# Performance work log

Measured on AMD Instinct MI355X. Metric: run time of the kernel, lower is better.

The kernel has to match this reference:

```python
import jax, jax.numpy as jnp
import numpy as np

B, S, LW = 64, 128, 20
CHAR_V, CHAR_E, CHAR_C = 100, 30, 30
WORD_V, WORD_E = 100000, 300
H, NC = 256, 25
F = WORD_E + CHAR_C  # 330


def setup_inputs() -> dict:
    key = jax.random.key(0)
    ks = jax.random.split(key, 16)
    u = lambda k, shape, s: jax.random.uniform(k, shape, jnp.float32, -s, s)
    sent = jax.random.randint(ks[0], (B, S), 0, WORD_V)
    word = jax.random.randint(ks[1], (B, S, LW), 0, CHAR_V)
    tag = jax.random.randint(ks[2], (B, S), 0, NC)
    lengths = jax.random.randint(ks[3], (B,), S // 2, S + 1)
    mask = jnp.arange(S)[None, :] < lengths[:, None]  # [B,S] bool, mask[:,0] all True

    word_table = u(ks[4], (WORD_V, WORD_E), 0.5)
    char_table = u(ks[5], (CHAR_V, CHAR_E), (3.0 / CHAR_E) ** 0.5)
    conv_w = u(ks[6], (CHAR_C, CHAR_E, 3), (6.0 / (CHAR_E * 3 + CHAR_C)) ** 0.5)
    conv_b = jnp.zeros((CHAR_C,), jnp.float32)

    def lstm_params(k):
        k1, k2 = jax.random.split(k)
        s_ih = (6.0 / (4 * H + F)) ** 0.5
        s_hh = (6.0 / (4 * H + H)) ** 0.5
        w_ih = u(k1, (4 * H, F), s_ih)
        w_hh = u(k2, (4 * H, H), s_hh)
        # b_ih + b_hh, each with forget-gate slice [H:2H] = 1.0 -> combined 2.0
        b = jnp.zeros((4 * H,), jnp.float32).at[H:2 * H].set(2.0)
        return w_ih, w_hh, b

    w_ih_f, w_hh_f, b_f = lstm_params(ks[7])
    w_ih_r, w_hh_r, b_r = lstm_params(ks[8])
    s_lin = (6.0 / (NC + 2 * H)) ** 0.5
    lin_w = u(ks[9], (NC, 2 * H), s_lin)
    lin_b = jnp.zeros((NC,), jnp.float32)
    start_t = u(ks[10], (NC,), 0.1)
    end_t = u(ks[11], (NC,), 0.1)
    trans = u(ks[12], (NC, NC), 0.1)
    return dict(word_table=word_table, char_table=char_table, conv_w=conv_w,
                conv_b=conv_b, w_ih_f=w_ih_f, w_hh_f=w_hh_f, b_f=b_f,
                w_ih_r=w_ih_r, w_hh_r=w_hh_r, b_r=b_r, lin_w=lin_w, lin_b=lin_b,
                start_t=start_t, end_t=end_t, trans=trans,
                sent=sent, word=word, tag=tag, mask=mask)


def _lstm_dir(x, w_ih, w_hh, b, reverse):
    # x: [B,S,F] -> precompute input projections time-major [S,B,4H]
    gx = jnp.einsum('bsf,gf->sbg', x, w_ih) + b
    bsz = x.shape[0]
    hs = w_hh.shape[1]

    def step(carry, g):
        h, c = carry
        g = g + h @ w_hh.T
        i, f, gg, o = jnp.split(g, 4, axis=-1)
        c = jax.nn.sigmoid(f) * c + jax.nn.sigmoid(i) * jnp.tanh(gg)
        h = jax.nn.sigmoid(o) * jnp.tanh(c)
        return (h, c), h

    init = (jnp.zeros((bsz, hs), x.dtype), jnp.zeros((bsz, hs), x.dtype))
    _, hseq = jax.lax.scan(step, init, gx, reverse=reverse)
    return hseq  # [S,B,H]


def _crf_nll(em, tg, mk, start_t, end_t, trans):
    # em: [S,B,C] emissions; tg: [S,B] int; mk: [S,B] float (mk[0]=1)
    bsz = em.shape[1]
    bidx = jnp.arange(bsz)
    # numerator: gold path score
    em_tag = jnp.take_along_axis(em, tg[..., None], axis=-1)[..., 0]   # [S,B]
    tr = trans[tg[:-1], tg[1:]]                                        # [S-1,B]
    score = start_t[tg[0]] + em_tag[0] + jnp.sum(mk[1:] * (tr + em_tag[1:]), axis=0)
    last = mk.sum(0).astype(jnp.int32) - 1
    score = score + end_t[tg[last, bidx]]
    # denominator: forward algorithm (logsumexp scan over time)
    alpha0 = start_t[None, :] + em[0]                                   # [B,C]

    def step(alpha, xs):
        em_t, mk_t = xs
        nxt = jax.nn.logsumexp(alpha[:, :, None] + trans[None, :, :] + em_t[:, None, :], axis=1)
        alpha = jnp.where(mk_t[:, None] > 0, nxt, alpha)
        return alpha, None

    alpha, _ = jax.lax.scan(step, alpha0, (em[1:], mk[1:]))
    logZ = jax.nn.logsumexp(alpha + end_t[None, :], axis=1)
    return -jnp.sum(score - logZ)  # model returns -log_likelihood (reduction='sum')


def reference(word_table, char_table, conv_w, conv_b, w_ih_f, w_hh_f, b_f,
              w_ih_r, w_hh_r, b_r, lin_w, lin_b, start_t, end_t, trans,
              sent, word, tag, mask):
    # --- char CNN encoder (dropout = identity in eval; no ReLU in original forward) ---
    ct = char_table.at[0].set(0.0)                      # padding_idx=0
    cemb = ct[word]                                     # [B,S,LW,E]
    x = cemb.reshape(B * S, LW, CHAR_E).transpose(0, 2, 1)  # [BS,E,LW]
    conv = jax.lax.conv_general_dilated(
        x, conv_w, window_strides=(1,), padding=[(1, 1)],
        dimension_numbers=('NCH', 'OIH', 'NCH')) + conv_b[None, :, None]
    char_feat = conv.max(axis=2).reshape(B, S, CHAR_C)  # global max-pool over chars
    # --- word embedding + concat ---
    wemb = word_table[sent]                             # [B,S,WORD_E]
    feat = jnp.concatenate([wemb, char_feat], axis=2)   # [B,S,F]
    # --- biLSTM ---
    hf = _lstm_dir(feat, w_ih_f, w_hh_f, b_f, reverse=False)
    hr = _lstm_dir(feat, w_ih_r, w_hh_r, b_r, reverse=True)
    h = jnp.concatenate([hf, hr], axis=-1)              # [S,B,2H] time-major
    em = h @ lin_w.T + lin_b                            # [S,B,NC]
    # --- CRF negative log-likelihood ---
    tg = tag.T
    mk = mask.T.astype(em.dtype)
    return _crf_nll(em, tg, mk, start_t, end_t, trans)
```

## Files before the change

### kernel.cpp

```cpp
#include <hip/hip_runtime.h>
#include <math.h>

#define B_  64
#define S_  128
#define LW_ 20
#define CHAR_E_ 30
#define CHAR_C_ 30
#define WORD_E_ 300
#define H_  256
#define NC_ 25
#define F_  330
#define KP_ 352
#define G4_ 1024
#define NG_ 2048

typedef __attribute__((ext_vector_type(8))) short short8;
typedef __attribute__((ext_vector_type(4))) float floatx4;
typedef __attribute__((ext_vector_type(8))) int int8v;

__device__ __forceinline__ unsigned int f2bf(float f){
    unsigned int u = __float_as_uint(f);
    u += 0x7FFFu + ((u>>16)&1u);
    return (u>>16) & 0xFFFFu;
}
__device__ __forceinline__ float bf2f(unsigned int v){ return __uint_as_float(v<<16); }

__device__ __forceinline__ float bfh(uint2 pk, int g){
    unsigned int w = (g < 2) ? pk.x : pk.y;
    return __uint_as_float((g & 1) ? (w & 0xffff0000u) : (w << 16));
}

__device__ __forceinline__ float sigf_(float x){ return __builtin_amdgcn_rcpf(1.0f+__expf(-x)); }
__device__ __forceinline__ float tanhf2_(float x){ return 1.0f - 2.0f*__builtin_amdgcn_rcpf(1.0f+__expf(2.0f*x)); }

__device__ __forceinline__ void gload16(const void* g, void* l){
    __builtin_amdgcn_global_load_lds((const __attribute__((address_space(1))) unsigned int*)g,
                                     (__attribute__((address_space(3))) unsigned int*)l, 16, 0, 0);
}

#define BAR_LDS() __asm__ volatile("s_waitcnt lgkmcnt(0)\n\ts_barrier" ::: "memory")

__global__ __launch_bounds__(256) void k_prep(const float* ct, const int* word,
        const float* cw, const float* cb, const float* wt, const int* sent,
        const float* wf, const float* wr, float* out,
        unsigned short* feat, unsigned short* wpack){
    __shared__ __align__(16) float x[8][32][20];
    int blk = blockIdx.x;
    int tid = threadIdx.x;
    if(blk < 1024){
        int tok0 = blk*8;
        for(int e = tid; e < 8*32*20; e += 256){
            int t  = e % 20;
            int ic = (e/20) & 31;
            int tl = e / 640;
            int id = word[(size_t)(tok0+tl)*LW_ + t];
            float v = 0.f;
            if(ic < CHAR_E_ && id != 0) v = ct[(size_t)id*CHAR_E_ + ic];
            x[tl][ic][t] = v;
        }
        __syncthreads();
        if(tid < 240){
            int tl = tid/30, oc = tid%30;
            float acc[22];
            #pragma unroll
            for(int q=0;q<22;q++) acc[q] = 0.f;
            for(int ic=0; ic<CHAR_E_; ic++){
                float w0 = cw[(oc*CHAR_E_+ic)*3+0];
                float w1 = cw[(oc*CHAR_E_+ic)*3+1];
                float w2 = cw[(oc*CHAR_E_+ic)*3+2];
                const float* xr = &x[tl][ic][0];
                #pragma unroll
                for(int t4=0;t4<5;t4++){
                    float4 v = ((const float4*)xr)[t4];
                    int t0 = t4*4;
                    acc[t0+2] += v.x*w0; acc[t0+1] += v.x*w1; acc[t0+0] += v.x*w2;
                    acc[t0+3] += v.y*w0; acc[t0+2] += v.y*w1; acc[t0+1] += v.y*w2;
                    acc[t0+4] += v.z*w0; acc[t0+3] += v.z*w1; acc[t0+2] += v.z*w2;
                    acc[t0+5] += v.w*w0; acc[t0+4] += v.w*w1; acc[t0+3] += v.w*w2;
                }
            }
            float m = -1e30f;
            #pragma unroll
            for(int t=0;t<20;t++){ float v = acc[t+1]; m = fmaxf(m, v); }
            m += cb[oc];
            feat[(size_t)(tok0+tl)*KP_ + WORD_E_ + oc] = (unsigned short)f2bf(m);
        }
    } else if(blk < 1024+2432){
        int idx = (blk-1024)*256 + tid;
        int n = idx / 76, e4 = idx % 76;
        if(e4 < 75){
            float4 v = ((const float4*)(wt + (size_t)sent[n]*WORD_E_))[e4];
            unsigned int lo = f2bf(v.x) | (f2bf(v.y)<<16);
            unsigned int hi = f2bf(v.z) | (f2bf(v.w)<<16);
            uint2 pr; pr.x = lo; pr.y = hi;
            *(uint2*)(feat + (size_t)n*KP_ + e4*4) = pr;
        } else {
            unsigned int* z = (unsigned int*)(feat + (size_t)n*KP_ + 330);
            #pragma unroll
            for(int q=0;q<11;q++) z[q] = 0;
        }
    } else if(blk < 6272){
        int i = (blk-3456)*256 + tid;
        int r = i / KP_, k = i % KP_;
        const float* src = (r < G4_) ? wf : wr;
        int rr = r & (G4_-1);
        wpack[i] = (k < F_) ? (unsigned short)f2bf(src[(size_t)rr*F_ + k]) : 0;
    } else {
        if(tid == 0) *out = 0.f;
    }
}

__global__ __launch_bounds__(256) void k_gemm(const unsigned short* A, const unsigned short* Bw,
                                              const float* bf, const float* br, unsigned short* gxb){
    __shared__ __align__(16) unsigned short As[128*32];
    __shared__ __align__(16) unsigned short Bs[128*32];
    int m0 = blockIdx.x*128, n0 = blockIdx.y*128;
    int tid = threadIdx.x;
    int w = tid>>6, lane = tid&63, q = lane>>4, l16 = lane&15;
    int wr = w>>1, wc = w&1;
    int srow0 = w*32 + (lane>>2);
    int scol  = (lane&3)*8;
    floatx4 acc[4][4];
    #pragma unroll
    for(int i=0;i<4;i++)
        #pragma unroll
        for(int j=0;j<4;j++) acc[i][j] = (floatx4){0.f,0.f,0.f,0.f};

    for(int k0=0; k0<KP_; k0+=32){
        __syncthreads();
        gload16(A  + (size_t)(m0+srow0   )*KP_ + k0 + scol, (unsigned short*)As + w*1024      );
        gload16(A  + (size_t)(m0+srow0+16)*KP_ + k0 + scol, (unsigned short*)As + w*1024 + 512);
        gload16(Bw + (size_t)(n0+srow0   )*KP_ + k0 + scol, (unsigned short*)Bs + w*1024      );
        gload16(Bw + (size_t)(n0+srow0+16)*KP_ + k0 + scol, (unsigned short*)Bs + w*1024 + 512);
        __asm__ volatile("s_waitcnt vmcnt(0)" ::: "memory");
        __syncthreads();
        short8 a_[4], b_[4];
        #pragma unroll
        for(int i=0;i<4;i++) a_[i] = *(const short8*)&As[(wr*64 + i*16 + l16)*32 + q*8];
        #pragma unroll
        for(int j=0;j<4;j++) b_[j] = *(const short8*)&Bs[(wc*64 + j*16 + l16)*32 + q*8];
        #pragma unroll
        for(int i=0;i<4;i++)
            #pragma unroll
            for(int j=0;j<4;j++)
                acc[i][j] = __builtin_amdgcn_mfma_f32_16x16x32_bf16(a_[i], b_[j], acc[i][j], 0,0,0);
    }
    #pragma unroll
    for(int j=0;j<4;j++){
        int n = n0 + wc*64 + j*16 + l16;
        int dirr = n >> 10, grow = n & 1023;
        float bias = dirr ? br[grow] : bf[grow];
        int gg  = grow >> 8;
        int ug  = grow & 255;
        int w16 = ug >> 4, u = ug & 15;
        int ubase = w16*128 + u*4 + gg;
        #pragma unroll
        for(int i=0;i<4;i++){
            int mb = m0 + wr*64 + i*16 + q*4;
            #pragma unroll
            for(int r=0;r<4;r++){
                int m = mb + r;
                int b = m >> 7, s = m & 127;
                size_t idx = ((size_t)((dirr*128 + s)*32 + (b>>1)))*2048
                           + (size_t)(ubase + (b&1)*64);
                gxb[idx] = (unsigned short)f2bf(acc[i][j][r] + bias);
            }
        }
    }
}

__device__ __forceinline__ void lstm_step16w(
    const unsigned char* hbb, unsigned char* hpub,
    float* wl, const int8v (*wreg)[2],
    int l16, int q, int lane,
    uint2 gg, float& cc, float* hs_ptr, const float inv_sc)
{
    floatx4 a[4];
    #pragma unroll
    for(int g=0; g<4; g++) a[g] = (floatx4){0.f,0.f,0.f,0.f};
    #pragma unroll
    for(int ki=0; ki<2; ki++){
        int8v hb = *(const int8v*)&hbb[l16*272 + ki*128 + q*32];
        #pragma unroll
        for(int g=0; g<4; g++)
            a[g] = __builtin_amdgcn_mfma_scale_f32_16x16x128_f8f6f4(wreg[g][ki], hb, a[g], 0,0,0,0x7F,0,0x7F);
    }
    if(l16 < 2){
        #pragma unroll
        for(int g=0; g<4; g++)
            *(floatx4*)&wl[g*32 + l16*16 + q*4] = a[g];
    }
    if(lane < 32){
        float iv = wl[0*32 + lane]*inv_sc + bfh(gg,0);
        float fv = wl[1*32 + lane]*inv_sc + bfh(gg,1);
        float gv = wl[2*32 + lane]*inv_sc + bfh(gg,2);
        float ov = wl[3*32 + lane]*inv_sc + bfh(gg,3);
        float cn = sigf_(fv)*cc + sigf_(iv)*tanhf2_(gv);
        cc = cn;
        float hv = sigf_(ov)*tanhf2_(cn);
        *hs_ptr = hv;
        unsigned int d8 = __builtin_amdgcn_cvt_pk_fp8_f32(hv*16.f, hv*16.f, 0u, false) & 0xFFu;
        *hpub = (unsigned char)d8;
    }
    BAR_LDS();
}

__global__ __launch_bounds__(1024,4) void k_lstm_all(const float* whhf, const float* whhr,
        const unsigned short* gxb, float* hseq)
{
    int bid = blockIdx.x;
    int dir = bid >> 5;
    int bgrp = bid & 31;
    int tid = threadIdx.x;
    int w16  = tid >> 6;
    int lane = tid & 63;
    int q    = lane >> 4;
    int l16  = lane & 15;
    int bb   = lane >> 4;
    int u    = lane & 15;

    __shared__ __align__(16) unsigned char hlds[2][16*272];
    __shared__ __align__(16) float wregion[16*128];

    const float* whh = dir ? whhr : whhf;

    int8v wreg[4][2];
    #pragma unroll
    for(int g=0; g<4; g++){
        const float* rp = whh + (size_t)(g*H_ + w16*16 + l16)*H_;
        #pragma unroll
        for(int ki=0; ki<2; ki++){
            const float* p = rp + ki*128 + q*32;
            int8v acc;
            #pragma unroll
            for(int wd=0; wd<8; wd++){
                unsigned int d = 0;
                d = __builtin_amdgcn_cvt_pk_fp8_f32(p[wd*4+0]*64.f, p[wd*4+1]*64.f, d, false);
                d = __builtin_amdgcn_cvt_pk_fp8_f32(p[wd*4+2]*64.f, p[wd*4+3]*64.f, d, true);
                acc[wd] = (int)d;
            }
            wreg[g][ki] = acc;
        }
    }

    for(int i = tid; i < 2*16*272/4; i += 1024) ((unsigned int*)hlds)[i] = 0;
    __syncthreads();

    const float inv_sc = 1.0f/1024.f;
    float cc = 0.f;

    int s0 = dir ? (S_-1) : 0;
    long gstep = dir ? -65536L : 65536L;
    const unsigned short* gp = gxb + ((size_t)((dir*128 + s0)*32 + bgrp))*2048 + w16*128 + lane*4;
    long hstep = dir ? -(long)(B_*H_) : (long)(B_*H_);
    float* hp = hseq + (((size_t)dir*S_ + s0)*B_ + bgrp*2 + bb)*H_ + w16*16 + u;

    float* wl = &wregion[w16*128];
    unsigned char* hpw0 = &hlds[0][bb*272 + w16*16 + u];
    unsigned char* hpw1 = &hlds[1][bb*272 + w16*16 + u];

    uint2 P = *(const uint2*)gp; gp += gstep;
    uint2 Q;

    for(int t=0; t<S_; t+=2){
        Q = *(const uint2*)gp; gp += gstep;
        lstm_step16w(&hlds[0][0], hpw1, wl, wreg, l16, q, lane, P, cc, hp, inv_sc);
        hp += hstep;
        P = *(const uint2*)gp; gp += gstep;
        lstm_step16w(&hlds[1][0], hpw0, wl, wreg, l16, q, lane, Q, cc, hp, inv_sc);
        hp += hstep;
    }
}

__global__ __launch_bounds__(256) void k_em(const float* hseq, const float* lw, const float* lb, float* em){
    __shared__ __align__(16) float hb[8][516];
    int sb0 = blockIdx.x*8;
    int tid = threadIdx.x;
    for(int i = tid; i < 1024; i += 256){
        int p = i >> 7, r = i & 127;
        int sb = sb0 + p, s = sb >> 6, b = sb & 63;
        const float* src = (r < 64) ? (hseq + (((size_t)0*S_+s)*B_+b)*H_ + r*4)
                                    : (hseq + (((size_t)1*S_+s)*B_+b)*H_ + (r-64)*4);
        *(float4*)&hb[p][r*4] = *(const float4*)src;
    }
    __syncthreads();
    if(tid < 200){
        int p = tid / 25, nc = tid % 25;
        const float4* wv = (const float4*)(lw + (size_t)nc*2*H_);
        const float4* hv = (const float4*)&hb[p][0];
        float acc = lb[nc];
        #pragma unroll 16
        for(int k=0;k<128;k++){ float4 a=hv[k], ww=wv[k]; acc += a.x*ww.x + a.y*ww.y + a.z*ww.z + a.w*ww.w; }
        em[(size_t)(sb0+p)*NC_ + nc] = acc;
    }
}

__global__ void k_crf(const float* em, const int* tag, const void* mask,
                      const float* st, const float* et, const float* tr, float* out){
    __shared__ float trs[NC_*NC_];
    int b = blockIdx.x, tid = threadIdx.x;
    for(int i=tid;i<NC_*NC_;i+=64) trs[i]=tr[i];
    unsigned int first = *(const unsigned int*)mask;
    int ml;
    if(first == 1u) ml = 0;
    else if(first == 0x3F800000u) ml = 2;
    else ml = 1;
    __syncthreads();

    float part = 0.f; int cnt = 0;
    for(int s = tid; s < S_; s += 64){
        float mkv;
        {
            int off = b*S_ + s;
            if(ml==0)      mkv = ((const int*)mask)[off] ? 1.f : 0.f;
            else if(ml==1) mkv = ((const unsigned char*)mask)[off] ? 1.f : 0.f;
            else           mkv = ((const float*)mask)[off];
        }
        cnt += (mkv != 0.f) ? 1 : 0;
        if(s == 0){
            int t0 = tag[b*S_];
            part += st[t0] + em[((size_t)0*B_ + b)*NC_ + t0];
        } else {
            int tp = tag[b*S_ + s-1], tc = tag[b*S_ + s];
            part += mkv * (trs[tp*NC_ + tc] + em[((size_t)s*B_ + b)*NC_ + tc]);
        }
    }
    for(int o=32;o>0;o>>=1){ part += __shfl_down(part, o); cnt += __shfl_down(cnt, o); }
    float score = 0.f;
    int len = __shfl(cnt, 0);
    float score0 = __shfl(part, 0);
    if(tid == 0) score = score0 + et[ tag[b*S_ + len-1] ];

    float Ecol[NC_];
    if(tid < NC_){
        #pragma unroll
        for(int i=0;i<NC_;i++) Ecol[i] = __expf(trs[i*NC_+tid]);
    } else {
        #pragma unroll
        for(int i=0;i<NC_;i++) Ecol[i] = 0.f;
    }

    float alpha = (tid < NC_) ? (st[tid] + em[((size_t)0*B_ + b)*NC_ + tid]) : -1e30f;
    float em_n = (tid < NC_) ? em[((size_t)1*B_ + b)*NC_ + tid] : 0.f;

    for(int s=1;s<S_;s++){
        float em_c = em_n;
        if(s+1 < S_) em_n = (tid < NC_) ? em[((size_t)(s+1)*B_ + b)*NC_ + tid] : 0.f;
        float mkv;
        {
            int off = b*S_ + s;
            if(ml==0)      mkv = ((const int*)mask)[off] ? 1.f : 0.f;
            else if(ml==1) mkv = ((const unsigned char*)mask)[off] ? 1.f : 0.f;
            else           mkv = ((const float*)mask)[off];
        }
        float v = alpha;
        #pragma unroll
        for(int o=16;o>0;o>>=1) v = fmaxf(v, __shfl_down(v, o));
        float m = __shfl(v, 0);
        float a = (tid < NC_) ? __expf(alpha - m) : 0.f;
        float S0 = 0.f, S1 = 0.f;
        #pragma unroll
        for(int i=0;i<24;i+=2){ S0 += __shfl(a, i) * Ecol[i]; S1 += __shfl(a, i+1) * Ecol[i+1]; }
        S0 += __shfl(a, 24) * Ecol[24];
        float nxt = m + __logf(S0 + S1) + em_c;
        if(tid < NC_ && mkv != 0.f) alpha = nxt;
    }

    float v = (tid < NC_) ? (alpha + et[tid]) : -1e30f;
    float m2 = v;
    #pragma unroll
    for(int o=16;o>0;o>>=1) m2 = fmaxf(m2, __shfl_down(m2, o));
    m2 = __shfl(m2, 0);
    float e = (tid < NC_) ? __expf(v - m2) : 0.f;
    #pragma unroll
    for(int o=16;o>0;o>>=1) e += __shfl_down(e, o);
    if(tid == 0){
        float logZ = m2 + __logf(e);
        atomicAdd(out, logZ - score);
    }
}

extern "C" void kernel_launch(void* const* d_in, const int* in_sizes, int n_in,
                              void* d_out, int out_size, void* d_ws, size_t ws_size,
                              hipStream_t stream) {
    const float* word_table = (const float*)d_in[0];
    const float* char_table = (const float*)d_in[1];
    const float* conv_w     = (const float*)d_in[2];
    const float* conv_b     = (const float*)d_in[3];
    const float* w_ih_f     = (const float*)d_in[4];
    const float* w_hh_f     = (const float*)d_in[5];
    const float* b_f        = (const float*)d_in[6];
    const float* w_ih_r     = (const float*)d_in[7];
    const float* w_hh_r     = (const float*)d_in[8];
    const float* b_r        = (const float*)d_in[9];
    const float* lin_w      = (const float*)d_in[10];
    const float* lin_b      = (const float*)d_in[11];
    const float* start_t    = (const float*)d_in[12];
    const float* end_t      = (const float*)d_in[13];
    const float* trans      = (const float*)d_in[14];
    const int*   sent       = (const int*)d_in[15];
    const int*   word       = (const int*)d_in[16];
    const int*   tag        = (const int*)d_in[17];
    const void*  mask       = d_in[18];
    float* out = (float*)d_out;

    char* ws = (char*)d_ws;
    unsigned short* feat  = (unsigned short*)ws;
    unsigned short* wpack = (unsigned short*)(ws + 5767168);
    unsigned short* gxb   = (unsigned short*)(ws + 5767168 + 1441792);
    float* hseq = (float*)(ws + 5767168 + 1441792 + 33554432);
    float* em   = (float*)(ws + 5767168 + 1441792 + 33554432 + 16777216);

    k_prep<<<dim3(6273), 256, 0, stream>>>(char_table, word, conv_w, conv_b,
                                           word_table, sent, w_ih_f, w_ih_r, out, feat, wpack);
    k_gemm<<<dim3(B_*S_/128, NG_/128), 256, 0, stream>>>(feat, wpack, b_f, b_r, gxb);
    k_lstm_all<<<dim3(64), 1024, 0, stream>>>(w_hh_f, w_hh_r, gxb, hseq);
    k_em<<<dim3(S_*B_/8), 256, 0, stream>>>(hseq, lin_w, lin_b, em);
    k_crf<<<dim3(B_), 64, 0, stream>>>(em, tag, mask, start_t, end_t, trans, out);
}
```

Measured before the change: 571.7 us.

## Fuse emission projection into CRF kernel and split LSTM MFMA accumulation chains

The emission linear layer is merged into the CRF kernel. Each of 64 blocks computes its batch's 128x25 emissions into LDS, which removes one launch and the global em round-trip. The LSTM step now uses two independent MFMA accumulator chains for the two K halves and sums them at the end, shortening the dependent MFMA chain on the serial critical path. The cost is that the emission compute runs on only 64 blocks instead of 1024, so that phase loses parallelism.

```diff
diff --git a/kernel.cpp b/kernel.cpp
--- a/kernel.cpp
+++ b/kernel.cpp
@@ -175,20 +175,22 @@
     int l16, int q, int lane,
     uint2 gg, float& cc, float* hs_ptr, const float inv_sc)
 {
-    floatx4 a[4];
-    #pragma unroll
-    for(int g=0; g<4; g++) a[g] = (floatx4){0.f,0.f,0.f,0.f};
-    #pragma unroll
-    for(int ki=0; ki<2; ki++){
-        int8v hb = *(const int8v*)&hbb[l16*272 + ki*128 + q*32];
-        #pragma unroll
-        for(int g=0; g<4; g++)
-            a[g] = __builtin_amdgcn_mfma_scale_f32_16x16x128_f8f6f4(wreg[g][ki], hb, a[g], 0,0,0,0x7F,0,0x7F);
+    int8v hb0 = *(const int8v*)&hbb[l16*272 + q*32];
+    int8v hb1 = *(const int8v*)&hbb[l16*272 + 128 + q*32];
+    floatx4 a0[4], a1[4];
+    #pragma unroll
+    for(int g=0; g<4; g++){ a0[g] = (floatx4){0.f,0.f,0.f,0.f}; a1[g] = a0[g]; }
+    #pragma unroll
+    for(int g=0; g<4; g++){
+        a0[g] = __builtin_amdgcn_mfma_scale_f32_16x16x128_f8f6f4(wreg[g][0], hb0, a0[g], 0,0,0,0x7F,0,0x7F);
+        a1[g] = __builtin_amdgcn_mfma_scale_f32_16x16x128_f8f6f4(wreg[g][1], hb1, a1[g], 0,0,0,0x7F,0,0x7F);
     }
     if(l16 < 2){
         #pragma unroll
-        for(int g=0; g<4; g++)
-            *(floatx4*)&wl[g*32 + l16*16 + q*4] = a[g];
+        for(int g=0; g<4; g++){
+            floatx4 s = a0[g] + a1[g];
+            *(floatx4*)&wl[g*32 + l16*16 + q*4] = s;
+        }
     }
     if(lane < 32){
         float iv = wl[0*32 + lane]*inv_sc + bfh(gg,0);
@@ -272,40 +274,44 @@
     }
 }
 
-__global__ __launch_bounds__(256) void k_em(const float* hseq, const float* lw, const float* lb, float* em){
-    __shared__ __align__(16) float hb[8][516];
-    int sb0 = blockIdx.x*8;
-    int tid = threadIdx.x;
-    for(int i = tid; i < 1024; i += 256){
-        int p = i >> 7, r = i & 127;
-        int sb = sb0 + p, s = sb >> 6, b = sb & 63;
-        const float* src = (r < 64) ? (hseq + (((size_t)0*S_+s)*B_+b)*H_ + r*4)
-                                    : (hseq + (((size_t)1*S_+s)*B_+b)*H_ + (r-64)*4);
-        *(float4*)&hb[p][r*4] = *(const float4*)src;
-    }
-    __syncthreads();
-    if(tid < 200){
-        int p = tid / 25, nc = tid % 25;
-        const float4* wv = (const float4*)(lw + (size_t)nc*2*H_);
-        const float4* hv = (const float4*)&hb[p][0];
-        float acc = lb[nc];
-        #pragma unroll 16
-        for(int k=0;k<128;k++){ float4 a=hv[k], ww=wv[k]; acc += a.x*ww.x + a.y*ww.y + a.z*ww.z + a.w*ww.w; }
-        em[(size_t)(sb0+p)*NC_ + nc] = acc;
-    }
-}
-
-__global__ void k_crf(const float* em, const int* tag, const void* mask,
-                      const float* st, const float* et, const float* tr, float* out){
+__global__ __launch_bounds__(256) void k_emcrf(const float* hseq, const float* lw, const float* lb,
+        const int* tag, const void* mask, const float* st, const float* et, const float* tr, float* out){
+    __shared__ __align__(16) float hst[8][516];
+    __shared__ float els[S_][26];
     __shared__ float trs[NC_*NC_];
     int b = blockIdx.x, tid = threadIdx.x;
-    for(int i=tid;i<NC_*NC_;i+=64) trs[i]=tr[i];
+    for(int i=tid;i<NC_*NC_;i+=256) trs[i]=tr[i];
+    int sl = tid >> 5;
+    int nc = tid & 31;
+    float lbv = (nc < NC_) ? lb[nc] : 0.f;
+    for(int c=0;c<16;c++){
+        int sbase = c*8;
+        __syncthreads();
+        for(int i = tid; i < 1024; i += 256){
+            int p = i >> 7, r = i & 127;
+            int s = sbase + p;
+            const float* src = (r < 64) ? (hseq + (((size_t)0*S_+s)*B_+b)*H_ + r*4)
+                                        : (hseq + (((size_t)1*S_+s)*B_+b)*H_ + (r-64)*4);
+            *(float4*)&hst[p][r*4] = *(const float4*)src;
+        }
+        __syncthreads();
+        if(nc < NC_){
+            const float4* wv = (const float4*)(lw + (size_t)nc*2*H_);
+            const float4* hv = (const float4*)&hst[sl][0];
+            float acc = lbv;
+            #pragma unroll 16
+            for(int k=0;k<128;k++){ float4 a=hv[k], ww=wv[k]; acc += a.x*ww.x + a.y*ww.y + a.z*ww.z + a.w*ww.w; }
+            els[sbase+sl][nc] = acc;
+        }
+    }
+    __syncthreads();
+    if(tid >= 64) return;
+
     unsigned int first = *(const unsigned int*)mask;
     int ml;
     if(first == 1u) ml = 0;
     else if(first == 0x3F800000u) ml = 2;
     else ml = 1;
-    __syncthreads();
 
     float part = 0.f; int cnt = 0;
     for(int s = tid; s < S_; s += 64){
@@ -319,10 +325,10 @@
         cnt += (mkv != 0.f) ? 1 : 0;
         if(s == 0){
             int t0 = tag[b*S_];
-            part += st[t0] + em[((size_t)0*B_ + b)*NC_ + t0];
+            part += st[t0] + els[0][t0];
         } else {
             int tp = tag[b*S_ + s-1], tc = tag[b*S_ + s];
-            part += mkv * (trs[tp*NC_ + tc] + em[((size_t)s*B_ + b)*NC_ + tc]);
+            part += mkv * (trs[tp*NC_ + tc] + els[s][tc]);
         }
     }
     for(int o=32;o>0;o>>=1){ part += __shfl_down(part, o); cnt += __shfl_down(cnt, o); }
@@ -340,12 +346,10 @@
         for(int i=0;i<NC_;i++) Ecol[i] = 0.f;
     }
 
-    float alpha = (tid < NC_) ? (st[tid] + em[((size_t)0*B_ + b)*NC_ + tid]) : -1e30f;
-    float em_n = (tid < NC_) ? em[((size_t)1*B_ + b)*NC_ + tid] : 0.f;
+    float alpha = (tid < NC_) ? (st[tid] + els[0][tid]) : -1e30f;
 
     for(int s=1;s<S_;s++){
-        float em_c = em_n;
-        if(s+1 < S_) em_n = (tid < NC_) ? em[((size_t)(s+1)*B_ + b)*NC_ + tid] : 0.f;
+        float em_c = (tid < NC_) ? els[s][tid] : 0.f;
         float mkv;
         {
             int off = b*S_ + s;
@@ -409,12 +413,10 @@
     unsigned short* wpack = (unsigned short*)(ws + 5767168);
     unsigned short* gxb   = (unsigned short*)(ws + 5767168 + 1441792);
     float* hseq = (float*)(ws + 5767168 + 1441792 + 33554432);
-    float* em   = (float*)(ws + 5767168 + 1441792 + 33554432 + 16777216);
 
     k_prep<<<dim3(6273), 256, 0, stream>>>(char_table, word, conv_w, conv_b,
                                            word_table, sent, w_ih_f, w_ih_r, out, feat, wpack);
     k_gemm<<<dim3(B_*S_/128, NG_/128), 256, 0, stream>>>(feat, wpack, b_f, b_r, gxb);
     k_lstm_all<<<dim3(64), 1024, 0, stream>>>(w_hh_f, w_hh_r, gxb, hseq);
-    k_em<<<dim3(S_*B_/8), 256, 0, stream>>>(hseq, lin_w, lin_b, em);
-    k_crf<<<dim3(B_), 64, 0, stream>>>(em, tag, mask, start_t, end_t, trans, out);
-}
+    k_emcrf<<<dim3(B_), 256, 0, stream>>>(hseq, lin_w, lin_b, tag, mask, start_t, end_t, trans, out);
+}
```

Result: slower. 742.8 us (+29.9%).
